# Kernel tuning notes

Measured on AMD Instinct MI355X. Metric: run time of the kernel, lower is better.

## Reference

```python
import jax, jax.numpy as jnp
import numpy as np

STRIDE = 1
MAX_STRIDE = 250  # 25 * 10 default


def setup_inputs() -> dict:
    key = jax.random.key(0)
    k1, k2 = jax.random.split(key)
    T = 1_000_000
    prediction = jax.random.normal(k1, (T,), dtype=jnp.float32)
    ground_truth = jax.random.normal(k2, (T,), dtype=jnp.float32)
    return {"prediction": prediction, "ground_truth": ground_truth}


def reference(prediction, ground_truth):
    T = prediction.shape[0]
    lags = jnp.arange(0, MAX_STRIDE, STRIDE)
    idx = jnp.arange(T)

    # ground-truth statistics are lag-independent
    mean_gt = jnp.mean(ground_truth)
    var_gt = jnp.var(ground_truth, ddof=1)  # torch.var is unbiased
    v_gt = ground_truth - mean_gt

    def ccc_at_lag(n):
        # shifted pred: n leading zeros followed by prediction[:-n]
        src = idx - n
        pred = jnp.where(src >= 0, prediction[jnp.clip(src, 0)], 0.0)
        mean_pred = jnp.mean(pred)
        var_pred = jnp.var(pred, ddof=1)
        cov = jnp.mean((pred - mean_pred) * v_gt)  # population covariance
        denom = var_gt + var_pred + (mean_gt - mean_pred) ** 2
        return 2.0 * cov / denom

    cccs = jax.vmap(ccc_at_lag)(lags)  # [n_lags]
    return 1.0 - jnp.mean(cccs)
```

## Files before the change

### kernel.cpp

```cpp
#include <hip/hip_runtime.h>
#include <hip/hip_bf16.h>


#define TC 4096
#define NTHR 512
#define NLAG 256
#define NUSED 250
#define NREP 16
#define GT4 (TC / 4 + 66)
#define GT4_A 584
#define PRED4 (TC / 4)
#define PRED4_A 512
#define STATREP_OFF (NREP * NLAG)
#define COUNTER_OFF (STATREP_OFF + NREP * 16)
#define NSUB 32
#define CHUNK 68

typedef float f2 __attribute__((ext_vector_type(2)));

__device__ __forceinline__ float4 ld_gt_sw(const float* s_gt, int i4) {
    int s = i4 ^ ((i4 >> 3) & 7);
    return *(const float4*)&s_gt[4 * s];
}

__device__ __forceinline__ void st_gt_sw(float* s_gt, int i4, float4 v) {
    int s = i4 ^ ((i4 >> 3) & 7);
    *(float4*)&s_gt[4 * s] = v;
}

__device__ __forceinline__ int pred_off(int i4) {
    return (i4 >> 4) * CHUNK + 4 * (i4 & 15);
}

__device__ __forceinline__ float ld_atomic(const float* p) {
    return __hip_atomic_load(p, __ATOMIC_RELAXED, __HIP_MEMORY_SCOPE_AGENT);
}

__device__ __forceinline__ void corr16(const float* __restrict__ s_gt,
                                       const float* __restrict__ pbase,
                                       int gi, f2* acc2) {
    f2 E[10], O[9];
    {
        float4 a = ld_gt_sw(s_gt, gi);
        float4 b = ld_gt_sw(s_gt, gi + 1);
        float4 d = ld_gt_sw(s_gt, gi + 2);
        float4 e = ld_gt_sw(s_gt, gi + 3);
        float4 f = ld_gt_sw(s_gt, gi + 4);
        E[0] = f2{a.x, a.y}; E[1] = f2{a.z, a.w};
        E[2] = f2{b.x, b.y}; E[3] = f2{b.z, b.w};
        E[4] = f2{d.x, d.y}; E[5] = f2{d.z, d.w};
        E[6] = f2{e.x, e.y}; E[7] = f2{e.z, e.w};
        E[8] = f2{f.x, f.y}; E[9] = f2{f.z, f.w};
        O[0] = f2{a.y, a.z}; O[1] = f2{a.w, b.x};
        O[2] = f2{b.y, b.z}; O[3] = f2{b.w, d.x};
        O[4] = f2{d.y, d.z}; O[5] = f2{d.w, e.x};
        O[6] = f2{e.y, e.z}; O[7] = f2{e.w, f.x};
        O[8] = f2{f.y, f.z};
    }
    #pragma unroll
    for (int it = 0; it < 16; ++it) {
        float4 nw = ld_gt_sw(s_gt, gi + 5 + it);
        float4 p = *(const float4*)&pbase[4 * it];
        f2 pA = f2{p.x, p.y}, pB = f2{p.z, p.w};
        #pragma unroll
        for (int m = 0; m < 8; ++m) {
            acc2[2 * m]     = __builtin_elementwise_fma(pA, E[m],     acc2[2 * m]);
            acc2[2 * m]     = __builtin_elementwise_fma(pB, E[m + 1], acc2[2 * m]);
            acc2[2 * m + 1] = __builtin_elementwise_fma(pA, O[m],     acc2[2 * m + 1]);
            acc2[2 * m + 1] = __builtin_elementwise_fma(pB, O[m + 1], acc2[2 * m + 1]);
        }
        float w19 = E[9].y;
        #pragma unroll
        for (int q = 0; q < 8; ++q) E[q] = E[q + 2];
        E[8] = f2{nw.x, nw.y}; E[9] = f2{nw.z, nw.w};
        #pragma unroll
        for (int q = 0; q < 7; ++q) O[q] = O[q + 2];
        O[7] = f2{w19, nw.x}; O[8] = f2{nw.y, nw.z};
    }
}

__global__ __launch_bounds__(NTHR) void ccc_fused(const float* __restrict__ pred,
                                                  const float* __restrict__ gt,
                                                  float* __restrict__ ws,
                                                  float* __restrict__ out,
                                                  int T, int nch) {
    __shared__ __align__(16) float s_pred[2 * NSUB * CHUNK];
    __shared__ __align__(16) float s_gt[GT4 * 4];
    __shared__ __align__(16) float s_acc[NSUB][NLAG];
    __shared__ float s_red[8][4];
    __shared__ float s_stats[4];
    __shared__ float s_sp64[64];
    __shared__ unsigned s_last;

    const int tid = threadIdx.x;
    const int c = blockIdx.x;
    const int j0 = c * TC;
    const bool interior = (j0 + 4 * GT4 <= T);

    float sp = 0.f, qp = 0.f, sg = 0.f, qg = 0.f;
    if (interior) {
        {
            float4 v = *(const float4*)&pred[j0 + 4 * tid];
            *(float4*)&s_pred[pred_off(tid)] = v;
            sp += v.x + v.y + v.z + v.w;
            qp += v.x * v.x + v.y * v.y + v.z * v.z + v.w * v.w;
        }
        for (int i4 = tid; i4 < GT4_A; i4 += NTHR) {
            float4 v = *(const float4*)&gt[j0 + 4 * i4];
            st_gt_sw(s_gt, i4, v);
            sg += v.x + v.y + v.z + v.w;
            qg += v.x * v.x + v.y * v.y + v.z * v.z + v.w * v.w;
        }
    } else {
        #pragma unroll 2
        for (int i4 = tid; i4 < PRED4; i4 += NTHR) {
            int g = j0 + 4 * i4;
            float4 v = make_float4(0.f, 0.f, 0.f, 0.f);
            if (g + 3 < T) v = *(const float4*)&pred[g];
            *(float4*)&s_pred[pred_off(i4)] = v;
            sp += v.x + v.y + v.z + v.w;
            qp += v.x * v.x + v.y * v.y + v.z * v.z + v.w * v.w;
        }
        #pragma unroll 2
        for (int i4 = tid; i4 < GT4; i4 += NTHR) {
            int g = j0 + 4 * i4;
            float4 v = make_float4(0.f, 0.f, 0.f, 0.f);
            if (g + 3 < T) v = *(const float4*)&gt[g];
            st_gt_sw(s_gt, i4, v);
            if (i4 < PRED4) {
                sg += v.x + v.y + v.z + v.w;
                qg += v.x * v.x + v.y * v.y + v.z * v.z + v.w * v.w;
            }
        }
    }
    __syncthreads();

    float4 pBp = make_float4(0.f, 0.f, 0.f, 0.f);
    float4 pBg = make_float4(0.f, 0.f, 0.f, 0.f);
    if (interior) {
        pBp = *(const float4*)&pred[j0 + 4 * (PRED4_A + tid)];
        if (tid < GT4 - GT4_A)
            pBg = *(const float4*)&gt[j0 + 4 * (GT4_A + tid)];
    }

    const int sub = tid >> 4;
    const int l = tid & 15;
    f2 acc2[16];
    #pragma unroll
    for (int k = 0; k < 16; ++k) acc2[k] = f2{0.f, 0.f};

    corr16(s_gt, &s_pred[sub * CHUNK], sub * 16 + 4 * l, acc2);

    if (interior) {
        *(float4*)&s_pred[pred_off(PRED4_A + tid)] = pBp;
        sp += pBp.x + pBp.y + pBp.z + pBp.w;
        qp += pBp.x * pBp.x + pBp.y * pBp.y + pBp.z * pBp.z + pBp.w * pBp.w;
        if (tid < GT4 - GT4_A) {
            st_gt_sw(s_gt, GT4_A + tid, pBg);
            if (GT4_A + tid < PRED4) {
                sg += pBg.x + pBg.y + pBg.z + pBg.w;
                qg += pBg.x * pBg.x + pBg.y * pBg.y + pBg.z * pBg.z + pBg.w * pBg.w;
            }
        }
    }
    __syncthreads();

    corr16(s_gt, &s_pred[(NSUB + sub) * CHUNK], 512 + sub * 16 + 4 * l, acc2);

    const int wv = tid >> 6, ln = tid & 63;
    #pragma unroll
    for (int off = 32; off > 0; off >>= 1) {
        sp += __shfl_down(sp, off, 64);
        qp += __shfl_down(qp, off, 64);
        sg += __shfl_down(sg, off, 64);
        qg += __shfl_down(qg, off, 64);
    }
    if (ln == 0) { s_red[wv][0] = sp; s_red[wv][1] = qp; s_red[wv][2] = sg; s_red[wv][3] = qg; }

    #pragma unroll
    for (int k = 0; k < 16; ++k)
        s_acc[sub][(l << 4) | (k ^ l)] = acc2[k].x + acc2[k].y;
    __syncthreads();

    const int rep = c & (NREP - 1);
    if (tid < NLAG) {
        float lagsum = 0.f;
        #pragma unroll
        for (int s2 = 0; s2 < NSUB; ++s2) lagsum += s_acc[s2][tid];
        int lag = (tid & 0xF0) | ((tid ^ (tid >> 4)) & 15);
        atomicAdd(&ws[rep * NLAG + lag], lagsum);
    }
    if (tid < 4) {
        float v = 0.f;
        #pragma unroll
        for (int w8 = 0; w8 < 8; ++w8) v += s_red[w8][tid];
        atomicAdd(&ws[STATREP_OFF + rep * 16 + tid], v);
    }

    __syncthreads();
    if (tid == 0) {
        unsigned* cnt = (unsigned*)(ws + COUNTER_OFF);
        unsigned old = __hip_atomic_fetch_add(cnt, 1u, __ATOMIC_RELAXED,
                                              __HIP_MEMORY_SCOPE_AGENT);
        unsigned want_poison = 0xAAAAAAAAu + (unsigned)(nch - 1);
        unsigned want_zero = (unsigned)(nch - 1);
        s_last = (old == want_poison || old == want_zero) ? 1u : 0u;
    }
    __syncthreads();
    if (!s_last) return;

    {
        const int lag = tid & 255, h = tid >> 8;
        float a = 0.f;
        #pragma unroll
        for (int r = 8 * h; r < 8 * h + 8; ++r) a += ld_atomic(&ws[r * NLAG + lag]);
        s_acc[h][lag] = a;
    }
    if (tid < 64) s_sp64[tid] = ld_atomic(&ws[STATREP_OFF + (tid >> 2) * 16 + (tid & 3)]);

    float tx = 0.f, tq = 0.f;
    if (tid < NLAG) {
        float t = pred[T - NLAG + tid];
        tx = t; tq = t * t;
    }
    #pragma unroll
    for (int d = 1; d < 64; d <<= 1) {
        float xs = __shfl_down(tx, d, 64);
        float qs = __shfl_down(tq, d, 64);
        if (ln + d < 64) { tx += xs; tq += qs; }
    }
    if (ln == 0) { s_red[wv][0] = tx; s_red[wv][1] = tq; }
    __syncthreads();

    if (tid < 4) {
        float s2 = 0.f;
        #pragma unroll
        for (int r = 0; r < 16; ++r) s2 += s_sp64[4 * r + tid];
        s_stats[tid] = s2;
    }
    if (tid < NLAG) {
        #pragma unroll
        for (int w2 = 1; w2 < 4; ++w2)
            if (w2 > wv) { tx += s_red[w2][0]; tq += s_red[w2][1]; }
        s_acc[2][tid] = tx;
        s_acc[3][tid] = tq;
    }
    __syncthreads();

    float v = 0.f;
    if (tid < NUSED) {
        const float Tf = (float)T;
        float sum_pred = s_stats[0], sumsq_pred = s_stats[1];
        float sum_gt = s_stats[2], sumsq_gt = s_stats[3];
        float mean_gt = sum_gt / Tf;
        float var_gt = (sumsq_gt - sum_gt * sum_gt / Tf) / (Tf - 1.f);
        float lagC = s_acc[0][tid] + s_acc[1][tid];
        float tail_s = (tid == 0) ? 0.f : s_acc[2][NLAG - tid];
        float tail_q = (tid == 0) ? 0.f : s_acc[3][NLAG - tid];
        float S = sum_pred - tail_s;
        float Q = sumsq_pred - tail_q;
        float mean_p = S / Tf;
        float var_p = (Q - S * S / Tf) / (Tf - 1.f);
        float cov = (lagC - mean_gt * S) / Tf;
        float dm = mean_gt - mean_p;
        v = 2.f * cov / (var_gt + var_p + dm * dm);
    }
    #pragma unroll
    for (int off = 32; off > 0; off >>= 1) v += __shfl_down(v, off, 64);
    if (ln == 0) s_red[wv][2] = v;
    __syncthreads();
    if (tid == 0) {
        float s2 = 0.f;
        #pragma unroll
        for (int w2 = 0; w2 < 8; ++w2) s2 += s_red[w2][2];
        out[0] = 1.f - s2 / (float)NUSED;
    }
}

extern "C" void kernel_launch(void* const* d_in, const int* in_sizes, int n_in,
                              void* d_out, int out_size, void* d_ws, size_t ws_size,
                              hipStream_t stream) {
    const float* pred = (const float*)d_in[0];
    const float* gt   = (const float*)d_in[1];
    float* out = (float*)d_out;
    float* ws  = (float*)d_ws;
    const int T = in_sizes[0];
    const int nch = (T + TC - 1) / TC;

    ccc_fused<<<nch, NTHR, 0, stream>>>(pred, gt, ws, out, T, nch);
}
```

Before: 69.52 us.

## Halve per-block chunk to one correlation pass and raise occupancy

Halves the per-block chunk from 4096 to 2048 samples. Each block now runs a single correlation pass, so the two-phase prefetch/second-pass pipeline and its extra barrier go away. The kernel also sets launch_bounds minimum blocks to 4 and reorders the FMA loop so the pA and pB products are split into two loops. This doubles the block count and the per-block accumulator reductions and atomics across blocks, betting on more resident waves and shorter blocks to hide latency.

```diff
diff --git a/kernel.cpp b/kernel.cpp
--- a/kernel.cpp
+++ b/kernel.cpp
@@ -2,15 +2,13 @@
 #include <hip/hip_bf16.h>
 
 
-#define TC 4096
+#define TC 2048
 #define NTHR 512
 #define NLAG 256
 #define NUSED 250
 #define NREP 16
 #define GT4 (TC / 4 + 66)
-#define GT4_A 584
 #define PRED4 (TC / 4)
-#define PRED4_A 512
 #define STATREP_OFF (NREP * NLAG)
 #define COUNTER_OFF (STATREP_OFF + NREP * 16)
 #define NSUB 32
@@ -64,9 +62,12 @@
         f2 pA = f2{p.x, p.y}, pB = f2{p.z, p.w};
         #pragma unroll
         for (int m = 0; m < 8; ++m) {
-            acc2[2 * m]     = __builtin_elementwise_fma(pA, E[m],     acc2[2 * m]);
+            acc2[2 * m]     = __builtin_elementwise_fma(pA, E[m], acc2[2 * m]);
+            acc2[2 * m + 1] = __builtin_elementwise_fma(pA, O[m], acc2[2 * m + 1]);
+        }
+        #pragma unroll
+        for (int m = 0; m < 8; ++m) {
             acc2[2 * m]     = __builtin_elementwise_fma(pB, E[m + 1], acc2[2 * m]);
-            acc2[2 * m + 1] = __builtin_elementwise_fma(pA, O[m],     acc2[2 * m + 1]);
             acc2[2 * m + 1] = __builtin_elementwise_fma(pB, O[m + 1], acc2[2 * m + 1]);
         }
         float w19 = E[9].y;
@@ -79,12 +80,12 @@
     }
 }
 
-__global__ __launch_bounds__(NTHR) void ccc_fused(const float* __restrict__ pred,
-                                                  const float* __restrict__ gt,
-                                                  float* __restrict__ ws,
-                                                  float* __restrict__ out,
-                                                  int T, int nch) {
-    __shared__ __align__(16) float s_pred[2 * NSUB * CHUNK];
+__global__ __launch_bounds__(NTHR, 4) void ccc_fused(const float* __restrict__ pred,
+                                                     const float* __restrict__ gt,
+                                                     float* __restrict__ ws,
+                                                     float* __restrict__ out,
+                                                     int T, int nch) {
+    __shared__ __align__(16) float s_pred[NSUB * CHUNK];
     __shared__ __align__(16) float s_gt[GT4 * 4];
     __shared__ __align__(16) float s_acc[NSUB][NLAG];
     __shared__ float s_red[8][4];
@@ -105,23 +106,23 @@
             sp += v.x + v.y + v.z + v.w;
             qp += v.x * v.x + v.y * v.y + v.z * v.z + v.w * v.w;
         }
-        for (int i4 = tid; i4 < GT4_A; i4 += NTHR) {
+        for (int i4 = tid; i4 < GT4; i4 += NTHR) {
             float4 v = *(const float4*)&gt[j0 + 4 * i4];
             st_gt_sw(s_gt, i4, v);
-            sg += v.x + v.y + v.z + v.w;
-            qg += v.x * v.x + v.y * v.y + v.z * v.z + v.w * v.w;
+            if (i4 < PRED4) {
+                sg += v.x + v.y + v.z + v.w;
+                qg += v.x * v.x + v.y * v.y + v.z * v.z + v.w * v.w;
+            }
         }
     } else {
-        #pragma unroll 2
-        for (int i4 = tid; i4 < PRED4; i4 += NTHR) {
-            int g = j0 + 4 * i4;
+        {
+            int g = j0 + 4 * tid;
             float4 v = make_float4(0.f, 0.f, 0.f, 0.f);
             if (g + 3 < T) v = *(const float4*)&pred[g];
-            *(float4*)&s_pred[pred_off(i4)] = v;
+            *(float4*)&s_pred[pred_off(tid)] = v;
             sp += v.x + v.y + v.z + v.w;
             qp += v.x * v.x + v.y * v.y + v.z * v.z + v.w * v.w;
         }
-        #pragma unroll 2
         for (int i4 = tid; i4 < GT4; i4 += NTHR) {
             int g = j0 + 4 * i4;
             float4 v = make_float4(0.f, 0.f, 0.f, 0.f);
@@ -135,14 +136,6 @@
     }
     __syncthreads();
 
-    float4 pBp = make_float4(0.f, 0.f, 0.f, 0.f);
-    float4 pBg = make_float4(0.f, 0.f, 0.f, 0.f);
-    if (interior) {
-        pBp = *(const float4*)&pred[j0 + 4 * (PRED4_A + tid)];
-        if (tid < GT4 - GT4_A)
-            pBg = *(const float4*)&gt[j0 + 4 * (GT4_A + tid)];
-    }
-
     const int sub = tid >> 4;
     const int l = tid & 15;
     f2 acc2[16];
@@ -150,22 +143,6 @@
     for (int k = 0; k < 16; ++k) acc2[k] = f2{0.f, 0.f};
 
     corr16(s_gt, &s_pred[sub * CHUNK], sub * 16 + 4 * l, acc2);
-
-    if (interior) {
-        *(float4*)&s_pred[pred_off(PRED4_A + tid)] = pBp;
-        sp += pBp.x + pBp.y + pBp.z + pBp.w;
-        qp += pBp.x * pBp.x + pBp.y * pBp.y + pBp.z * pBp.z + pBp.w * pBp.w;
-        if (tid < GT4 - GT4_A) {
-            st_gt_sw(s_gt, GT4_A + tid, pBg);
-            if (GT4_A + tid < PRED4) {
-                sg += pBg.x + pBg.y + pBg.z + pBg.w;
-                qg += pBg.x * pBg.x + pBg.y * pBg.y + pBg.z * pBg.z + pBg.w * pBg.w;
-            }
-        }
-    }
-    __syncthreads();
-
-    corr16(s_gt, &s_pred[(NSUB + sub) * CHUNK], 512 + sub * 16 + 4 * l, acc2);
 
     const int wv = tid >> 6, ln = tid & 63;
     #pragma unroll
```

Result: slower. 91.76 us (+32.0%).
